# Performance work log

Measured on AMD Instinct MI355X. Metric: run time of the kernel, lower is better.

## Reference

```python
import jax, jax.numpy as jnp
import numpy as np

BITS = 8
BOUND = 2.0 ** (BITS - 1) - 1.0  # 127, symmetric int8 bound
EPS = 1e-6


def fake_quant(x, scale):
    """Symmetric fake quantization with straight-through estimator."""
    q = jnp.clip(jnp.round(x * scale), -BOUND, BOUND) / scale
    return x + jax.lax.stop_gradient(q - x)


def dense_aqt(x, w, b, mask):
    """AQT-style quantized dense: per-tensor input scale (masked stats),
    per-output-channel weight scale, int8-range fake quant, float GEMM.
    x: [N, Cin], w: [Cin, Cout], b: [Cout], mask: [N, 1]."""
    x_max = jnp.max(jnp.abs(x * mask))                       # masked per-tensor stat
    sx = BOUND / jnp.maximum(x_max, EPS)
    w_max = jnp.max(jnp.abs(w), axis=0, keepdims=True)        # [1, Cout]
    sw = BOUND / jnp.maximum(w_max, EPS)
    xq = fake_quant(x, sx)
    wq = fake_quant(w, sw)
    return jnp.matmul(xq, wq) + b


def setup_inputs() -> dict:
    key = jax.random.key(0)
    k1, k2, k3 = jax.random.split(key, 3)
    B, S, C, H = 4, 2048, 1024, 4096
    inputs = jax.random.normal(k1, (B, S, C), dtype=jnp.float32)
    padding_mask = jnp.ones((B, S, 1), dtype=jnp.float32)
    W1 = jax.random.normal(k2, (C, H), dtype=jnp.float32) * (1.0 / np.sqrt(C))
    b1 = jnp.zeros((H,), dtype=jnp.float32)
    W2 = jax.random.normal(k3, (H, C), dtype=jnp.float32) * (1.0 / np.sqrt(H))
    b2 = jnp.zeros((C,), dtype=jnp.float32)
    return {"inputs": inputs, "padding_mask": padding_mask,
            "W1": W1, "b1": b1, "W2": W2, "b2": b2}


def reference(inputs, padding_mask, W1, b1, W2, b2):
    B, S, C = inputs.shape
    x = inputs.reshape(B * S, C)
    m = padding_mask.reshape(B * S, 1)
    h = jax.nn.relu(dense_aqt(x, W1, b1, m))   # dropout is no-op (deterministic)
    out = dense_aqt(h, W2, b2, m)              # dropout is no-op (deterministic)
    return out.reshape(B, S, C)
```

## Files before the change

### kernel.cpp

```cpp
#include <hip/hip_runtime.h>
#include <hip/hip_fp16.h>
#include <stdint.h>


#define EPSQ 1e-6f
typedef int v4i __attribute__((ext_vector_type(4)));
typedef int v16i __attribute__((ext_vector_type(16)));

__device__ __forceinline__ void async16(const int8_t* g, int8_t* l) {
  __builtin_amdgcn_global_load_lds(
      (const __attribute__((address_space(1))) void*)g,
      (__attribute__((address_space(3))) void*)l, 16, 0, 0);
}
__device__ __forceinline__ unsigned short f2h(float f) {
  __half h = __float2half(f);
  return *(unsigned short*)&h;
}
__device__ __forceinline__ float4 max4(float4 m, float4 v) {
  m.x = fmaxf(m.x, fabsf(v.x)); m.y = fmaxf(m.y, fabsf(v.y));
  m.z = fmaxf(m.z, fabsf(v.z)); m.w = fmaxf(m.w, fabsf(v.w));
  return m;
}
__device__ __forceinline__ unsigned qmb(float x, float s) {
  return __float_as_uint(fmaf(x, s, 12582912.0f)) & 0xffu;
}
__device__ __forceinline__ unsigned q4f(float4 f, float s) {
  return qmb(f.x, s) | (qmb(f.y, s) << 8) | (qmb(f.z, s) << 16) |
         (__float_as_uint(fmaf(f.w, s, 12582912.0f)) << 24);
}
__device__ __forceinline__ unsigned q4h(unsigned ua, unsigned ub,
                                        __half2 s2, __half2 m2) {
  __half2 ha = __hfma2(*(__half2*)&ua, s2, m2);
  __half2 hb = __hfma2(*(__half2*)&ub, s2, m2);
  unsigned va = *(unsigned*)&ha, vb = *(unsigned*)&hb;
#if __has_builtin(__builtin_amdgcn_perm)
  return __builtin_amdgcn_perm(vb, va, 0x06040200u);
#else
  return (va & 0xffu) | ((va >> 8) & 0xff00u) |
         ((vb & 0xffu) << 16) | (((vb >> 8) & 0xff00u) << 16);
#endif
}

__global__ __launch_bounds__(256) void k_stats(
    const float* __restrict__ x, const float* __restrict__ mask,
    const float* __restrict__ W1, const float* __restrict__ W2,
    float* __restrict__ pmaxX, float* __restrict__ pcm1, float* __restrict__ pcm2) {
  const int bx = blockIdx.x, tid = threadIdx.x;
  if (bx < 64) {
    const int sp = bx & 15, cg = bx >> 4;
    const int col = cg * 1024 + tid * 4;
    float4 m = {0.f, 0.f, 0.f, 0.f};
#pragma unroll 8
    for (int r = 0; r < 64; ++r)
      m = max4(m, *(const float4*)(W1 + (size_t)(sp * 64 + r) * 4096 + col));
    *(float4*)(pcm1 + sp * 4096 + col) = m;
  } else if (bx < 128) {
    const int sp = bx - 64;
    const int col = tid * 4;
    float4 m = {0.f, 0.f, 0.f, 0.f};
#pragma unroll 8
    for (int r = 0; r < 64; ++r)
      m = max4(m, *(const float4*)(W2 + (size_t)(sp * 64 + r) * 1024 + col));
    *(float4*)(pcm2 + sp * 1024 + col) = m;
  } else {
    __shared__ float red[4];
    const int b = bx - 128;
    float lmax = 0.f;
    for (int c = b * 256 + tid; c < 1048576; c += 262144) {
      size_t idx = (size_t)c * 8;
      float mk = fabsf(mask[idx >> 10]);
      float4 m4 = {0.f, 0.f, 0.f, 0.f};
      m4 = max4(m4, *(const float4*)(x + idx));
      m4 = max4(m4, *(const float4*)(x + idx + 4));
      lmax = fmaxf(lmax, fmaxf(fmaxf(m4.x, m4.y), fmaxf(m4.z, m4.w)) * mk);
    }
    for (int s = 32; s; s >>= 1) lmax = fmaxf(lmax, __shfl_down(lmax, s));
    if ((tid & 63) == 0) red[tid >> 6] = lmax;
    __syncthreads();
    if (tid == 0)
      pmaxX[b] = fmaxf(fmaxf(red[0], red[1]), fmaxf(red[2], red[3]));
  }
}

__global__ __launch_bounds__(256) void k_quant(
    const float* __restrict__ x, const float* __restrict__ W1, const float* __restrict__ W2,
    const float* __restrict__ pmaxX, const float* __restrict__ pcm1, const float* __restrict__ pcm2,
    int8_t* __restrict__ qx, int8_t* __restrict__ qw1, int8_t* __restrict__ qw2,
    float* __restrict__ cm1, float* __restrict__ cm2, float* __restrict__ scG) {
  const int bx = blockIdx.x, tid = threadIdx.x;
  if (bx < 2048) {
    __shared__ float red[4];
    float v = fmaxf(fmaxf(pmaxX[tid], pmaxX[tid + 256]),
                    fmaxf(pmaxX[tid + 512], pmaxX[tid + 768]));
    for (int s = 32; s; s >>= 1) v = fmaxf(v, __shfl_down(v, s));
    if ((tid & 63) == 0) red[tid >> 6] = v;
    __syncthreads();
    const float xmax = fmaxf(fmaxf(red[0], red[1]), fmaxf(red[2], red[3]));
    if (bx == 0 && tid == 0) scG[0] = xmax;
    const float s = 127.0f / fmaxf(xmax, EPSQ);
    const int wave = tid >> 6, lane = tid & 63;
    const int f = bx * 4 + wave;
    const int r = (f >> 5) * 32 + (lane & 31);
    const int k = (f & 31) * 32 + (lane >> 5) * 16;
    const float4* src = (const float4*)(x + (size_t)r * 1024 + k);
    uint4 o;
    o.x = q4f(src[0], s); o.y = q4f(src[1], s);
    o.z = q4f(src[2], s); o.w = q4f(src[3], s);
    *(uint4*)(qx + (size_t)f * 1024 + lane * 16) = o;
  } else if (bx < 2304) {
    int id = (bx - 2048) * 256 + tid;
    int n4 = id & 1023, kc = id >> 10;
    const int col = n4 * 4;
    float4 cm = {0.f, 0.f, 0.f, 0.f};
#pragma unroll
    for (int sp = 0; sp < 16; ++sp) {
      float4 p = *(const float4*)(pcm1 + sp * 4096 + col);
      cm.x = fmaxf(cm.x, p.x); cm.y = fmaxf(cm.y, p.y);
      cm.z = fmaxf(cm.z, p.z); cm.w = fmaxf(cm.w, p.w);
    }
    if (kc == 0) *(float4*)(cm1 + col) = cm;
    const float s0 = 127.0f / fmaxf(cm.x, EPSQ), s1 = 127.0f / fmaxf(cm.y, EPSQ);
    const float s2 = 127.0f / fmaxf(cm.z, EPSQ), s3 = 127.0f / fmaxf(cm.w, EPSQ);
    union { int8_t p[16]; uint4 v; } u0, u1, u2, u3;
#pragma unroll
    for (int j = 0; j < 16; ++j) {
      float4 f = *(const float4*)(W1 + (size_t)(kc * 16 + j) * 4096 + col);
      u0.p[j] = (int8_t)qmb(f.x, s0); u1.p[j] = (int8_t)qmb(f.y, s1);
      u2.p[j] = (int8_t)qmb(f.z, s2); u3.p[j] = (int8_t)qmb(f.w, s3);
    }
    int8_t* base = qw1 + ((size_t)(col >> 5) * 32 + (kc >> 1)) * 1024 +
                   (kc & 1) * 512 + (col & 31) * 16;
    *(uint4*)(base) = u0.v;      *(uint4*)(base + 16) = u1.v;
    *(uint4*)(base + 32) = u2.v; *(uint4*)(base + 48) = u3.v;
  } else {
    int id = (bx - 2304) * 256 + tid;
    int n4 = id & 255, kc = id >> 8;
    const int col = n4 * 4;
    float4 cm = {0.f, 0.f, 0.f, 0.f};
#pragma unroll
    for (int sp = 0; sp < 64; ++sp) {
      float4 p = *(const float4*)(pcm2 + sp * 1024 + col);
      cm.x = fmaxf(cm.x, p.x); cm.y = fmaxf(cm.y, p.y);
      cm.z = fmaxf(cm.z, p.z); cm.w = fmaxf(cm.w, p.w);
    }
    if (kc == 0) *(float4*)(cm2 + col) = cm;
    const float s0 = 127.0f / fmaxf(cm.x, EPSQ), s1 = 127.0f / fmaxf(cm.y, EPSQ);
    const float s2 = 127.0f / fmaxf(cm.z, EPSQ), s3 = 127.0f / fmaxf(cm.w, EPSQ);
    union { int8_t p[16]; uint4 v; } u0, u1, u2, u3;
#pragma unroll
    for (int j = 0; j < 16; ++j) {
      float4 f = *(const float4*)(W2 + (size_t)(kc * 16 + j) * 1024 + col);
      u0.p[j] = (int8_t)qmb(f.x, s0); u1.p[j] = (int8_t)qmb(f.y, s1);
      u2.p[j] = (int8_t)qmb(f.z, s2); u3.p[j] = (int8_t)qmb(f.w, s3);
    }
    int8_t* base = qw2 + ((size_t)(col >> 5) * 128 + (kc >> 1)) * 1024 +
                   (kc & 1) * 512 + (col & 31) * 16;
    *(uint4*)(base) = u0.v;      *(uint4*)(base + 16) = u1.v;
    *(uint4*)(base + 32) = u2.v; *(uint4*)(base + 48) = u3.v;
  }
}

__global__ __launch_bounds__(512, 4) void gemm1(
    const int8_t* __restrict__ A, const int8_t* __restrict__ Bt,
    const float* __restrict__ sxp, const float* __restrict__ cmax,
    const float* __restrict__ bias, const float* __restrict__ mask,
    unsigned short* __restrict__ hfrag, float* __restrict__ pmaxH) {
  constexpr int NST = 16;
  constexpr int BUF = 24576;
  __shared__ __align__(16) int8_t smem[3 * BUF];
  const int tid = threadIdx.x;
  const int wave = tid >> 6, lane = tid & 63;

  const int bid = blockIdx.x;
  const int xcd = bid & 7, sl = bid >> 3;
  const int m0 = (xcd * 4 + (sl & 3)) * 256;
  const int n0 = (sl >> 2) * 128;

  v16i acc[2][2] = {};

  const int8_t* gA = A  + ((size_t)((m0 >> 5) + wave) * 32) * 1024 + lane * 16;
  const int8_t* gB = Bt + ((size_t)((n0 >> 5) + (wave & 3)) * 32 + (wave >> 2)) * 1024
                     + lane * 16;
  const int dAo = wave * 1024 + lane * 16;
  const int dBo = 16384 + ((wave >> 2) * 4 + (wave & 3)) * 1024 + lane * 16;

  async16(gA,        smem + dAo);
  async16(gA + 1024, smem + dAo + 8192);
  async16(gB,        smem + dBo);
  async16(gA + 2048, smem + BUF + dAo);
  async16(gA + 3072, smem + BUF + dAo + 8192);
  async16(gB + 2048, smem + BUF + dBo);
  asm volatile("s_waitcnt vmcnt(3)" ::: "memory");
  __builtin_amdgcn_s_barrier();
  __builtin_amdgcn_sched_barrier(0);

  const int mI = (wave & 3) * 2, nI = (wave >> 2) * 2;
#pragma unroll
  for (int kb = 0; kb < NST; ++kb) {
    const int co = (kb % 3) * BUF;
    if (kb + 2 < NST) {
      const int po = ((kb + 2) % 3) * BUF;
      async16(gA + (kb + 2) * 2048,        smem + po + dAo);
      async16(gA + (kb + 2) * 2048 + 1024, smem + po + dAo + 8192);
      async16(gB + (kb + 2) * 2048,        smem + po + dBo);
    }
    __builtin_amdgcn_sched_barrier(0);
#pragma unroll
    for (int kc = 0; kc < 2; ++kc) {
      v4i af0 = *(const v4i*)(smem + co + (kc * 8 + mI) * 1024 + lane * 16);
      v4i af1 = *(const v4i*)(smem + co + (kc * 8 + mI + 1) * 1024 + lane * 16);
      v4i bf0 = *(const v4i*)(smem + co + 16384 + (kc * 4 + nI) * 1024 + lane * 16);
      v4i bf1 = *(const v4i*)(smem + co + 16384 + (kc * 4 + nI + 1) * 1024 + lane * 16);
      acc[0][0] = __builtin_amdgcn_mfma_i32_32x32x32_i8(af0, bf0, acc[0][0], 0, 0, 0);
      acc[0][1] = __builtin_amdgcn_mfma_i32_32x32x32_i8(af0, bf1, acc[0][1], 0, 0, 0);
      acc[1][0] = __builtin_amdgcn_mfma_i32_32x32x32_i8(af1, bf0, acc[1][0], 0, 0, 0);
      acc[1][1] = __builtin_amdgcn_mfma_i32_32x32x32_i8(af1, bf1, acc[1][1], 0, 0, 0);
    }
    if (kb + 1 < NST) {
      asm volatile("s_waitcnt lgkmcnt(0)" ::: "memory");
      if (kb + 2 < NST)
        asm volatile("s_waitcnt vmcnt(3)" ::: "memory");
      else
        asm volatile("s_waitcnt vmcnt(0)" ::: "memory");
      __builtin_amdgcn_s_barrier();
      __builtin_amdgcn_sched_barrier(0);
    }
  }

  const float asc = fmaxf(sxp[0], EPSQ) * (1.0f / 127.0f);
  const int cl = lane & 31;
  const int rbase = 4 * (lane >> 5);
  const int wr = wave & 3, wc = wave >> 2;
  float bsc[2], bv[2];
#pragma unroll
  for (int nt = 0; nt < 2; ++nt) {
    const int col = n0 + wc * 64 + nt * 32 + cl;
    bsc[nt] = fmaxf(cmax[col], EPSQ) * (1.0f / 127.0f) * asc;
    bv[nt] = bias[col];
  }
  const int hwoff = (cl >> 4) * 512 + (cl & 15);
  float lmax = 0.f;
#pragma unroll
  for (int mt = 0; mt < 2; ++mt) {
    const int rowbase = m0 + wr * 64 + mt * 32;
    const size_t rowblk = (size_t)(rowbase >> 5);
#pragma unroll
    for (int g = 0; g < 4; ++g)
#pragma unroll
      for (int r2 = 0; r2 < 4; ++r2) {
        const int rloc = g * 8 + r2 + rbase;
        const float mk = fabsf(mask[rowbase + rloc]);
#pragma unroll
        for (int nt = 0; nt < 2; ++nt) {
          const size_t kblk = (size_t)((n0 + wc * 64 + nt * 32) >> 5);
          float v = (float)acc[mt][nt][g * 4 + r2] * bsc[nt] + bv[nt];
          v = fmaxf(v, 0.f);
          hfrag[(rowblk * 128 + kblk) * 1024 + hwoff + rloc * 16] = f2h(v);
          lmax = fmaxf(lmax, v * mk);
        }
      }
  }
  for (int s = 32; s; s >>= 1) lmax = fmaxf(lmax, __shfl_down(lmax, s));
  __syncthreads();
  float* redf = (float*)smem;
  if (lane == 0) redf[wave] = lmax;
  __syncthreads();
  if (tid == 0) {
    float r = redf[0];
#pragma unroll
    for (int j = 1; j < 8; ++j) r = fmaxf(r, redf[j]);
    pmaxH[bid] = r;
  }
}

__global__ __launch_bounds__(256, 2) void gemm2(
    const unsigned short* __restrict__ hfrag, const int8_t* __restrict__ Bt,
    const float* __restrict__ pmaxH, const float* __restrict__ cmax,
    const float* __restrict__ bias, float* __restrict__ out) {
  __shared__ __align__(16) int8_t smem[32768];
  int8_t* const lsA = smem;
  int8_t* const lsB = smem + 16384;
  const int tid = threadIdx.x;
  const int wave = tid >> 6, lane = tid & 63;

  float* red = (float*)smem;
  float v = 0.f;
#pragma unroll
  for (int j = 0; j < 4; ++j) v = fmaxf(v, pmaxH[tid + 256 * j]);
  for (int s = 32; s; s >>= 1) v = fmaxf(v, __shfl_down(v, s));
  if (lane == 0) red[wave] = v;
  __syncthreads();
  const float hmax = fmaxf(fmaxf(red[0], red[1]), fmaxf(red[2], red[3]));
  __syncthreads();
  const float asc = fmaxf(hmax, EPSQ) * (1.0f / 127.0f);
  const __half sh = __float2half_rn(127.0f / fmaxf(hmax, EPSQ));
  const __half2 s2 = __halves2half2(sh, sh);
  const __half mh = __float2half_rn(1536.0f);
  const __half2 m2 = __halves2half2(mh, mh);

  const int bid = blockIdx.x;
  const int xcd = bid & 7, slot = bid >> 3;
  const int m0 = ((xcd << 3) + (slot >> 3)) * 128;
  const int n0 = (slot & 7) * 128;

  v16i acc[2][2] = {};

  const uint4* hA = (const uint4*)hfrag;
  const size_t aBase = ((size_t)((m0 >> 5) + wave) * 128) * 128 + lane * 2;
  const int8_t* gB = Bt + ((size_t)((n0 >> 5) + wave) * 128) * 1024 + lane * 16;
  int8_t* const dA0 = lsA + (0 * 4 + wave) * 1024 + lane * 16;
  int8_t* const dA1 = lsA + (1 * 4 + wave) * 1024 + lane * 16;
  int8_t* const dB0 = lsB + (0 * 4 + wave) * 1024 + lane * 16;
  int8_t* const dB1 = lsB + (1 * 4 + wave) * 1024 + lane * 16;

  const int nsteps = 64;
  const int mI = (wave & 1) * 2, nI = (wave >> 1) * 2;

  uint4 s0a0 = {}, s0a1 = {}, s0c0 = {}, s0c1 = {};
  uint4 s1a0 = {}, s1a1 = {}, s1c0 = {}, s1c1 = {};

  {
    uint4 a0 = hA[aBase], a1 = hA[aBase + 1];
    uint4 c0 = hA[aBase + 128], c1 = hA[aBase + 129];
    async16(gB, dB0);
    async16(gB + 1024, dB1);
    __builtin_amdgcn_sched_barrier(0);
    s1a0 = hA[aBase + 2 * 128]; s1a1 = hA[aBase + 2 * 128 + 1];
    s1c0 = hA[aBase + 3 * 128]; s1c1 = hA[aBase + 3 * 128 + 1];
    uint4 o;
    o.x = q4h(a0.x, a0.y, s2, m2); o.y = q4h(a0.z, a0.w, s2, m2);
    o.z = q4h(a1.x, a1.y, s2, m2); o.w = q4h(a1.z, a1.w, s2, m2);
    *(uint4*)dA0 = o;
    o.x = q4h(c0.x, c0.y, s2, m2); o.y = q4h(c0.z, c0.w, s2, m2);
    o.z = q4h(c1.x, c1.y, s2, m2); o.w = q4h(c1.z, c1.w, s2, m2);
    *(uint4*)dA1 = o;
  }
  asm volatile("s_waitcnt lgkmcnt(0)" ::: "memory");
  asm volatile("s_waitcnt vmcnt(4)" ::: "memory");
  __builtin_amdgcn_s_barrier();
  __builtin_amdgcn_sched_barrier(0);

#pragma unroll 2
  for (int kb = 0; kb < nsteps; ++kb) {
    const int cur = kb & 1;
    const int co = cur * 8192, po = co ^ 8192;
    const bool more = (kb + 1 < nsteps);
    const bool deep = (kb + 2 < nsteps);
    if (more) {
      async16(gB + (size_t)((kb + 1) * 2) * 1024, dB0 + po);
      async16(gB + (size_t)((kb + 1) * 2 + 1) * 1024, dB1 + po);
      __builtin_amdgcn_sched_barrier(0);
      if (deep) {
        const size_t ai = aBase + (size_t)((kb + 2) * 2) * 128;
        if (cur) { s1a0 = hA[ai]; s1a1 = hA[ai + 1];
                   s1c0 = hA[ai + 128]; s1c1 = hA[ai + 129]; }
        else     { s0a0 = hA[ai]; s0a1 = hA[ai + 1];
                   s0c0 = hA[ai + 128]; s0c1 = hA[ai + 129]; }
      }
    }
#pragma unroll
    for (int kc = 0; kc < 2; ++kc) {
      v4i af0 = *(const v4i*)(lsA + co + (kc * 4 + mI) * 1024 + lane * 16);
      v4i af1 = *(const v4i*)(lsA + co + (kc * 4 + mI + 1) * 1024 + lane * 16);
      v4i bf0 = *(const v4i*)(lsB + co + (kc * 4 + nI) * 1024 + lane * 16);
      v4i bf1 = *(const v4i*)(lsB + co + (kc * 4 + nI + 1) * 1024 + lane * 16);
      acc[0][0] = __builtin_amdgcn_mfma_i32_32x32x32_i8(af0, bf0, acc[0][0], 0, 0, 0);
      acc[0][1] = __builtin_amdgcn_mfma_i32_32x32x32_i8(af0, bf1, acc[0][1], 0, 0, 0);
      acc[1][0] = __builtin_amdgcn_mfma_i32_32x32x32_i8(af1, bf0, acc[1][0], 0, 0, 0);
      acc[1][1] = __builtin_amdgcn_mfma_i32_32x32x32_i8(af1, bf1, acc[1][1], 0, 0, 0);
    }
    if (more) {
      const uint4 pa0 = cur ? s0a0 : s1a0, pa1 = cur ? s0a1 : s1a1;
      const uint4 pc0 = cur ? s0c0 : s1c0, pc1 = cur ? s0c1 : s1c1;
      uint4 o;
      o.x = q4h(pa0.x, pa0.y, s2, m2); o.y = q4h(pa0.z, pa0.w, s2, m2);
      o.z = q4h(pa1.x, pa1.y, s2, m2); o.w = q4h(pa1.z, pa1.w, s2, m2);
      *(uint4*)(dA0 + po) = o;
      o.x = q4h(pc0.x, pc0.y, s2, m2); o.y = q4h(pc0.z, pc0.w, s2, m2);
      o.z = q4h(pc1.x, pc1.y, s2, m2); o.w = q4h(pc1.z, pc1.w, s2, m2);
      *(uint4*)(dA1 + po) = o;
      asm volatile("s_waitcnt lgkmcnt(0)" ::: "memory");
      if (deep) asm volatile("s_waitcnt vmcnt(4)" ::: "memory");
      else      asm volatile("s_waitcnt vmcnt(0)" ::: "memory");
      __builtin_amdgcn_s_barrier();
      __builtin_amdgcn_sched_barrier(0);
    }
  }

  const int cl = lane & 31;
  const int rbase = 4 * (lane >> 5);
  const int wr = wave & 1, wc = wave >> 1;
  float bsc[2], bv[2];
  int colv[2];
#pragma unroll
  for (int nt = 0; nt < 2; ++nt) {
    colv[nt] = n0 + wc * 64 + nt * 32 + cl;
    bsc[nt] = fmaxf(cmax[colv[nt]], EPSQ) * (1.0f / 127.0f) * asc;
    bv[nt] = bias[colv[nt]];
  }
#pragma unroll
  for (int mt = 0; mt < 2; ++mt)
#pragma unroll
    for (int g = 0; g < 4; ++g)
#pragma unroll
      for (int r2 = 0; r2 < 4; ++r2) {
        const int row = m0 + wr * 64 + mt * 32 + g * 8 + r2 + rbase;
#pragma unroll
        for (int nt = 0; nt < 2; ++nt)
          out[(size_t)row * 1024 + colv[nt]] =
              (float)acc[mt][nt][g * 4 + r2] * bsc[nt] + bv[nt];
      }
}

extern "C" void kernel_launch(void* const* d_in, const int* in_sizes, int n_in,
                              void* d_out, int out_size, void* d_ws, size_t ws_size,
                              hipStream_t stream) {
  const float* x  = (const float*)d_in[0];
  const float* mk = (const float*)d_in[1];
  const float* W1 = (const float*)d_in[2];
  const float* b1 = (const float*)d_in[3];
  const float* W2 = (const float*)d_in[4];
  const float* b2 = (const float*)d_in[5];
  float* out = (float*)d_out;

  float* scG   = (float*)d_ws;
  float* pmaxX = scG + 8;
  float* pmaxH = pmaxX + 1024;
  float* pcm1  = pmaxH + 2048;
  float* pcm2  = pcm1 + 65536;
  float* cm1   = pcm2 + 65536;
  float* cm2   = cm1 + 4096;
  int8_t* qx  = (int8_t*)(cm2 + 1024);
  int8_t* qw1 = qx  + (size_t)8192 * 1024;
  int8_t* qw2 = qw1 + (size_t)4096 * 1024;
  unsigned short* h = (unsigned short*)(qw2 + (size_t)1024 * 4096);

  k_stats<<<1152, 256, 0, stream>>>(x, mk, W1, W2, pmaxX, pcm1, pcm2);
  k_quant<<<2560, 256, 0, stream>>>(x, W1, W2, pmaxX, pcm1, pcm2,
                                    qx, qw1, qw2, cm1, cm2, scG);
  gemm1<<<1024, 512, 0, stream>>>(qx, qw1, scG, cm1, b1, mk, h, pmaxH);
  gemm2<<<512, 256, 0, stream>>>(h, qw2, pmaxH, cm2, b2, out);
}
```

Measured before the change: 228.0 us.

## Deepen gemm2 pipeline to a four-stage LDS ring with split-phase barriers

The second int8 GEMM moves from double-buffered LDS to a four-slot ring. B tiles are prefetched two steps ahead via global_load_lds, and A activations are loaded into registers three steps ahead, then quantized into LDS two steps ahead. Each k-step is split into two halves with their own barrier, and the MFMA groups are wrapped in s_setprio. The aim is to hide global-load latency and barrier stalls behind MFMA work. In exchange, LDS per block grows to 64KB, which may limit occupancy, and the vmcnt ordering is implicit and fragile.

```diff
diff --git a/kernel.cpp b/kernel.cpp
--- a/kernel.cpp
+++ b/kernel.cpp
@@ -277,9 +277,8 @@
     const unsigned short* __restrict__ hfrag, const int8_t* __restrict__ Bt,
     const float* __restrict__ pmaxH, const float* __restrict__ cmax,
     const float* __restrict__ bias, float* __restrict__ out) {
-  __shared__ __align__(16) int8_t smem[32768];
-  int8_t* const lsA = smem;
-  int8_t* const lsB = smem + 16384;
+  constexpr int NST = 64;
+  __shared__ __align__(16) int8_t smem[4 * 16384];
   const int tid = threadIdx.x;
   const int wave = tid >> 6, lane = tid & 63;
 
@@ -308,81 +307,104 @@
   const uint4* hA = (const uint4*)hfrag;
   const size_t aBase = ((size_t)((m0 >> 5) + wave) * 128) * 128 + lane * 2;
   const int8_t* gB = Bt + ((size_t)((n0 >> 5) + wave) * 128) * 1024 + lane * 16;
-  int8_t* const dA0 = lsA + (0 * 4 + wave) * 1024 + lane * 16;
-  int8_t* const dA1 = lsA + (1 * 4 + wave) * 1024 + lane * 16;
-  int8_t* const dB0 = lsB + (0 * 4 + wave) * 1024 + lane * 16;
-  int8_t* const dB1 = lsB + (1 * 4 + wave) * 1024 + lane * 16;
-
-  const int nsteps = 64;
+  const int dA0o = (0 * 4 + wave) * 1024 + lane * 16;
+  const int dA1o = (1 * 4 + wave) * 1024 + lane * 16;
+  const int dB0o = 8192 + (0 * 4 + wave) * 1024 + lane * 16;
+  const int dB1o = 8192 + (1 * 4 + wave) * 1024 + lane * 16;
   const int mI = (wave & 1) * 2, nI = (wave >> 1) * 2;
 
-  uint4 s0a0 = {}, s0a1 = {}, s0c0 = {}, s0c1 = {};
-  uint4 s1a0 = {}, s1a1 = {}, s1c0 = {}, s1c1 = {};
+  uint4 ra0, ra1, rc0, rc1;
 
   {
     uint4 a0 = hA[aBase], a1 = hA[aBase + 1];
     uint4 c0 = hA[aBase + 128], c1 = hA[aBase + 129];
-    async16(gB, dB0);
-    async16(gB + 1024, dB1);
-    __builtin_amdgcn_sched_barrier(0);
-    s1a0 = hA[aBase + 2 * 128]; s1a1 = hA[aBase + 2 * 128 + 1];
-    s1c0 = hA[aBase + 3 * 128]; s1c1 = hA[aBase + 3 * 128 + 1];
+    __builtin_amdgcn_sched_barrier(0);
+    async16(gB,            smem + dB0o);
+    async16(gB + 1024,     smem + dB1o);
+    async16(gB + 2 * 1024, smem + 16384 + dB0o);
+    async16(gB + 3 * 1024, smem + 16384 + dB1o);
+    __builtin_amdgcn_sched_barrier(0);
     uint4 o;
     o.x = q4h(a0.x, a0.y, s2, m2); o.y = q4h(a0.z, a0.w, s2, m2);
     o.z = q4h(a1.x, a1.y, s2, m2); o.w = q4h(a1.z, a1.w, s2, m2);
-    *(uint4*)dA0 = o;
+    *(uint4*)(smem + dA0o) = o;
     o.x = q4h(c0.x, c0.y, s2, m2); o.y = q4h(c0.z, c0.w, s2, m2);
     o.z = q4h(c1.x, c1.y, s2, m2); o.w = q4h(c1.z, c1.w, s2, m2);
-    *(uint4*)dA1 = o;
+    *(uint4*)(smem + dA1o) = o;
+    __builtin_amdgcn_sched_barrier(0);
+    a0 = hA[aBase + 2 * 128]; a1 = hA[aBase + 2 * 128 + 1];
+    c0 = hA[aBase + 3 * 128]; c1 = hA[aBase + 3 * 128 + 1];
+    __builtin_amdgcn_sched_barrier(0);
+    o.x = q4h(a0.x, a0.y, s2, m2); o.y = q4h(a0.z, a0.w, s2, m2);
+    o.z = q4h(a1.x, a1.y, s2, m2); o.w = q4h(a1.z, a1.w, s2, m2);
+    *(uint4*)(smem + 16384 + dA0o) = o;
+    o.x = q4h(c0.x, c0.y, s2, m2); o.y = q4h(c0.z, c0.w, s2, m2);
+    o.z = q4h(c1.x, c1.y, s2, m2); o.w = q4h(c1.z, c1.w, s2, m2);
+    *(uint4*)(smem + 16384 + dA1o) = o;
+    __builtin_amdgcn_sched_barrier(0);
+    ra0 = hA[aBase + 4 * 128]; ra1 = hA[aBase + 4 * 128 + 1];
+    rc0 = hA[aBase + 5 * 128]; rc1 = hA[aBase + 5 * 128 + 1];
   }
   asm volatile("s_waitcnt lgkmcnt(0)" ::: "memory");
-  asm volatile("s_waitcnt vmcnt(4)" ::: "memory");
-  __builtin_amdgcn_s_barrier();
   __builtin_amdgcn_sched_barrier(0);
 
-#pragma unroll 2
-  for (int kb = 0; kb < nsteps; ++kb) {
-    const int cur = kb & 1;
-    const int co = cur * 8192, po = co ^ 8192;
-    const bool more = (kb + 1 < nsteps);
-    const bool deep = (kb + 2 < nsteps);
-    if (more) {
-      async16(gB + (size_t)((kb + 1) * 2) * 1024, dB0 + po);
-      async16(gB + (size_t)((kb + 1) * 2 + 1) * 1024, dB1 + po);
+#pragma unroll 4
+  for (int kb = 0; kb < NST; ++kb) {
+    const int cb = (kb & 3) * 16384;
+    const int nb2 = ((kb + 2) & 3) * 16384;
+    __builtin_amdgcn_s_barrier();
+    __builtin_amdgcn_sched_barrier(0);
+    {
+      v4i af0 = *(const v4i*)(smem + cb + (0 * 4 + mI) * 1024 + lane * 16);
+      v4i af1 = *(const v4i*)(smem + cb + (0 * 4 + mI + 1) * 1024 + lane * 16);
+      v4i bf0 = *(const v4i*)(smem + cb + 8192 + (0 * 4 + nI) * 1024 + lane * 16);
+      v4i bf1 = *(const v4i*)(smem + cb + 8192 + (0 * 4 + nI + 1) * 1024 + lane * 16);
+      if (kb + 2 < NST) {
+        async16(gB + (size_t)((kb + 2) * 2) * 1024,     smem + nb2 + dB0o);
+        async16(gB + (size_t)((kb + 2) * 2 + 1) * 1024, smem + nb2 + dB1o);
+      }
+      asm volatile("s_waitcnt lgkmcnt(0)" ::: "memory");
       __builtin_amdgcn_sched_barrier(0);
-      if (deep) {
-        const size_t ai = aBase + (size_t)((kb + 2) * 2) * 128;
-        if (cur) { s1a0 = hA[ai]; s1a1 = hA[ai + 1];
-                   s1c0 = hA[ai + 128]; s1c1 = hA[ai + 129]; }
-        else     { s0a0 = hA[ai]; s0a1 = hA[ai + 1];
-                   s0c0 = hA[ai + 128]; s0c1 = hA[ai + 129]; }
-      }
-    }
-#pragma unroll
-    for (int kc = 0; kc < 2; ++kc) {
-      v4i af0 = *(const v4i*)(lsA + co + (kc * 4 + mI) * 1024 + lane * 16);
-      v4i af1 = *(const v4i*)(lsA + co + (kc * 4 + mI + 1) * 1024 + lane * 16);
-      v4i bf0 = *(const v4i*)(lsB + co + (kc * 4 + nI) * 1024 + lane * 16);
-      v4i bf1 = *(const v4i*)(lsB + co + (kc * 4 + nI + 1) * 1024 + lane * 16);
+      __builtin_amdgcn_s_setprio(1);
       acc[0][0] = __builtin_amdgcn_mfma_i32_32x32x32_i8(af0, bf0, acc[0][0], 0, 0, 0);
       acc[0][1] = __builtin_amdgcn_mfma_i32_32x32x32_i8(af0, bf1, acc[0][1], 0, 0, 0);
       acc[1][0] = __builtin_amdgcn_mfma_i32_32x32x32_i8(af1, bf0, acc[1][0], 0, 0, 0);
       acc[1][1] = __builtin_amdgcn_mfma_i32_32x32x32_i8(af1, bf1, acc[1][1], 0, 0, 0);
-    }
-    if (more) {
-      const uint4 pa0 = cur ? s0a0 : s1a0, pa1 = cur ? s0a1 : s1a1;
-      const uint4 pc0 = cur ? s0c0 : s1c0, pc1 = cur ? s0c1 : s1c1;
-      uint4 o;
-      o.x = q4h(pa0.x, pa0.y, s2, m2); o.y = q4h(pa0.z, pa0.w, s2, m2);
-      o.z = q4h(pa1.x, pa1.y, s2, m2); o.w = q4h(pa1.z, pa1.w, s2, m2);
-      *(uint4*)(dA0 + po) = o;
-      o.x = q4h(pc0.x, pc0.y, s2, m2); o.y = q4h(pc0.z, pc0.w, s2, m2);
-      o.z = q4h(pc1.x, pc1.y, s2, m2); o.w = q4h(pc1.z, pc1.w, s2, m2);
-      *(uint4*)(dA1 + po) = o;
+      __builtin_amdgcn_s_setprio(0);
+      __builtin_amdgcn_sched_barrier(0);
+    }
+    __builtin_amdgcn_s_barrier();
+    __builtin_amdgcn_sched_barrier(0);
+    {
+      v4i af0 = *(const v4i*)(smem + cb + (1 * 4 + mI) * 1024 + lane * 16);
+      v4i af1 = *(const v4i*)(smem + cb + (1 * 4 + mI + 1) * 1024 + lane * 16);
+      v4i bf0 = *(const v4i*)(smem + cb + 8192 + (1 * 4 + nI) * 1024 + lane * 16);
+      v4i bf1 = *(const v4i*)(smem + cb + 8192 + (1 * 4 + nI + 1) * 1024 + lane * 16);
+      if (kb + 2 < NST) {
+        uint4 o;
+        o.x = q4h(ra0.x, ra0.y, s2, m2); o.y = q4h(ra0.z, ra0.w, s2, m2);
+        o.z = q4h(ra1.x, ra1.y, s2, m2); o.w = q4h(ra1.z, ra1.w, s2, m2);
+        *(uint4*)(smem + nb2 + dA0o) = o;
+        o.x = q4h(rc0.x, rc0.y, s2, m2); o.y = q4h(rc0.z, rc0.w, s2, m2);
+        o.z = q4h(rc1.x, rc1.y, s2, m2); o.w = q4h(rc1.z, rc1.w, s2, m2);
+        *(uint4*)(smem + nb2 + dA1o) = o;
+        __builtin_amdgcn_sched_barrier(0);
+        if (kb + 3 < NST) {
+          const size_t ai = aBase + (size_t)((kb + 3) * 2) * 128;
+          ra0 = hA[ai]; ra1 = hA[ai + 1];
+          rc0 = hA[ai + 128]; rc1 = hA[ai + 129];
+        }
+      } else {
+        asm volatile("s_waitcnt vmcnt(0)" ::: "memory");
+      }
       asm volatile("s_waitcnt lgkmcnt(0)" ::: "memory");
-      if (deep) asm volatile("s_waitcnt vmcnt(4)" ::: "memory");
-      else      asm volatile("s_waitcnt vmcnt(0)" ::: "memory");
-      __builtin_amdgcn_s_barrier();
+      __builtin_amdgcn_sched_barrier(0);
+      __builtin_amdgcn_s_setprio(1);
+      acc[0][0] = __builtin_amdgcn_mfma_i32_32x32x32_i8(af0, bf0, acc[0][0], 0, 0, 0);
+      acc[0][1] = __builtin_amdgcn_mfma_i32_32x32x32_i8(af0, bf1, acc[0][1], 0, 0, 0);
+      acc[1][0] = __builtin_amdgcn_mfma_i32_32x32x32_i8(af1, bf0, acc[1][0], 0, 0, 0);
+      acc[1][1] = __builtin_amdgcn_mfma_i32_32x32x32_i8(af1, bf1, acc[1][1], 0, 0, 0);
+      __builtin_amdgcn_s_setprio(0);
       __builtin_amdgcn_sched_barrier(0);
     }
   }
```

Result: no change. 229.9 us (+0.8%).

## Load A fragments straight to registers, stage only B in LDS

Applied to the files above, without the earlier changes.

In both GEMM kernels, each wave now loads its A-operand fragments directly from global memory into registers, double-buffered across k-steps. Only the shared B tile is staged in LDS, which shrinks LDS use and removes the A LDS writes and reads and their lgkm waits. gemm2 now quantizes its fp16 A fragments in registers right before the MFMAs and gives each wave a 32x128 strip, with occupancy raised to 3 blocks. s_setprio hints wrap the MFMA groups. The trade-off is more register pressure and no LDS sharing of A, which is fine because each A fragment is used by a single wave.

```diff
diff --git a/kernel.cpp b/kernel.cpp
--- a/kernel.cpp
+++ b/kernel.cpp
@@ -166,8 +166,7 @@
     const float* __restrict__ bias, const float* __restrict__ mask,
     unsigned short* __restrict__ hfrag, float* __restrict__ pmaxH) {
   constexpr int NST = 16;
-  constexpr int BUF = 24576;
-  __shared__ __align__(16) int8_t smem[3 * BUF];
+  __shared__ __align__(16) int8_t smem[2 * 8192];
   const int tid = threadIdx.x;
   const int wave = tid >> 6, lane = tid & 63;
 
@@ -175,53 +174,69 @@
   const int xcd = bid & 7, sl = bid >> 3;
   const int m0 = (xcd * 4 + (sl & 3)) * 256;
   const int n0 = (sl >> 2) * 128;
+  const int wr = wave & 3, wc = wave >> 2;
 
   v16i acc[2][2] = {};
 
-  const int8_t* gA = A  + ((size_t)((m0 >> 5) + wave) * 32) * 1024 + lane * 16;
-  const int8_t* gB = Bt + ((size_t)((n0 >> 5) + (wave & 3)) * 32 + (wave >> 2)) * 1024
-                     + lane * 16;
-  const int dAo = wave * 1024 + lane * 16;
-  const int dBo = 16384 + ((wave >> 2) * 4 + (wave & 3)) * 1024 + lane * 16;
-
-  async16(gA,        smem + dAo);
-  async16(gA + 1024, smem + dAo + 8192);
-  async16(gB,        smem + dBo);
-  async16(gA + 2048, smem + BUF + dAo);
-  async16(gA + 3072, smem + BUF + dAo + 8192);
-  async16(gB + 2048, smem + BUF + dBo);
-  asm volatile("s_waitcnt vmcnt(3)" ::: "memory");
+  const int8_t* gA = A + ((size_t)((m0 >> 5) + wr * 2) * 32) * 1024 + lane * 16;
+  const int kcS = wave >> 2, nbS = wave & 3;
+  const int8_t* gB = Bt + ((size_t)((n0 >> 5) + nbS) * 32 + kcS) * 1024 + lane * 16;
+  const int dBo = wave * 1024 + lane * 16;
+  const int rdo = wc * 2048 + lane * 16;
+
+  v4i aP0, aP1, aP2, aP3, aQ0, aQ1, aQ2, aQ3;
+
+  async16(gB, smem + dBo);
+  __builtin_amdgcn_sched_barrier(0);
+  aP0 = *(const v4i*)(gA);
+  aP1 = *(const v4i*)(gA + 1024);
+  aP2 = *(const v4i*)(gA + 32768);
+  aP3 = *(const v4i*)(gA + 32768 + 1024);
+  asm volatile("s_waitcnt vmcnt(4)" ::: "memory");
   __builtin_amdgcn_s_barrier();
   __builtin_amdgcn_sched_barrier(0);
 
-  const int mI = (wave & 3) * 2, nI = (wave >> 2) * 2;
-#pragma unroll
+#pragma unroll 2
   for (int kb = 0; kb < NST; ++kb) {
-    const int co = (kb % 3) * BUF;
-    if (kb + 2 < NST) {
-      const int po = ((kb + 2) % 3) * BUF;
-      async16(gA + (kb + 2) * 2048,        smem + po + dAo);
-      async16(gA + (kb + 2) * 2048 + 1024, smem + po + dAo + 8192);
-      async16(gB + (kb + 2) * 2048,        smem + po + dBo);
-    }
-    __builtin_amdgcn_sched_barrier(0);
-#pragma unroll
-    for (int kc = 0; kc < 2; ++kc) {
-      v4i af0 = *(const v4i*)(smem + co + (kc * 8 + mI) * 1024 + lane * 16);
-      v4i af1 = *(const v4i*)(smem + co + (kc * 8 + mI + 1) * 1024 + lane * 16);
-      v4i bf0 = *(const v4i*)(smem + co + 16384 + (kc * 4 + nI) * 1024 + lane * 16);
-      v4i bf1 = *(const v4i*)(smem + co + 16384 + (kc * 4 + nI + 1) * 1024 + lane * 16);
-      acc[0][0] = __builtin_amdgcn_mfma_i32_32x32x32_i8(af0, bf0, acc[0][0], 0, 0, 0);
-      acc[0][1] = __builtin_amdgcn_mfma_i32_32x32x32_i8(af0, bf1, acc[0][1], 0, 0, 0);
-      acc[1][0] = __builtin_amdgcn_mfma_i32_32x32x32_i8(af1, bf0, acc[1][0], 0, 0, 0);
-      acc[1][1] = __builtin_amdgcn_mfma_i32_32x32x32_i8(af1, bf1, acc[1][1], 0, 0, 0);
-    }
-    if (kb + 1 < NST) {
-      asm volatile("s_waitcnt lgkmcnt(0)" ::: "memory");
-      if (kb + 2 < NST)
-        asm volatile("s_waitcnt vmcnt(3)" ::: "memory");
-      else
-        asm volatile("s_waitcnt vmcnt(0)" ::: "memory");
+    const int slot = (kb & 1) * 8192, nslot = slot ^ 8192;
+    const bool more = (kb + 1 < NST);
+    if (more) {
+      async16(gB + (size_t)(kb + 1) * 2048, smem + nslot + dBo);
+      __builtin_amdgcn_sched_barrier(0);
+      const int8_t* ga = gA + (size_t)(kb + 1) * 2048;
+      if (kb & 1) {
+        aP0 = *(const v4i*)(ga);         aP1 = *(const v4i*)(ga + 1024);
+        aP2 = *(const v4i*)(ga + 32768); aP3 = *(const v4i*)(ga + 32768 + 1024);
+      } else {
+        aQ0 = *(const v4i*)(ga);         aQ1 = *(const v4i*)(ga + 1024);
+        aQ2 = *(const v4i*)(ga + 32768); aQ3 = *(const v4i*)(ga + 32768 + 1024);
+      }
+      __builtin_amdgcn_sched_barrier(0);
+    }
+    {
+      const v4i a00 = (kb & 1) ? aQ0 : aP0;
+      const v4i a01 = (kb & 1) ? aQ1 : aP1;
+      const v4i a10 = (kb & 1) ? aQ2 : aP2;
+      const v4i a11 = (kb & 1) ? aQ3 : aP3;
+      v4i b0 = *(const v4i*)(smem + slot + rdo);
+      v4i b1 = *(const v4i*)(smem + slot + rdo + 1024);
+      __builtin_amdgcn_s_setprio(1);
+      acc[0][0] = __builtin_amdgcn_mfma_i32_32x32x32_i8(a00, b0, acc[0][0], 0, 0, 0);
+      acc[0][1] = __builtin_amdgcn_mfma_i32_32x32x32_i8(a00, b1, acc[0][1], 0, 0, 0);
+      acc[1][0] = __builtin_amdgcn_mfma_i32_32x32x32_i8(a10, b0, acc[1][0], 0, 0, 0);
+      acc[1][1] = __builtin_amdgcn_mfma_i32_32x32x32_i8(a10, b1, acc[1][1], 0, 0, 0);
+      __builtin_amdgcn_s_setprio(0);
+      v4i b2 = *(const v4i*)(smem + slot + 4096 + rdo);
+      v4i b3 = *(const v4i*)(smem + slot + 4096 + rdo + 1024);
+      __builtin_amdgcn_s_setprio(1);
+      acc[0][0] = __builtin_amdgcn_mfma_i32_32x32x32_i8(a01, b2, acc[0][0], 0, 0, 0);
+      acc[0][1] = __builtin_amdgcn_mfma_i32_32x32x32_i8(a01, b3, acc[0][1], 0, 0, 0);
+      acc[1][0] = __builtin_amdgcn_mfma_i32_32x32x32_i8(a11, b2, acc[1][0], 0, 0, 0);
+      acc[1][1] = __builtin_amdgcn_mfma_i32_32x32x32_i8(a11, b3, acc[1][1], 0, 0, 0);
+      __builtin_amdgcn_s_setprio(0);
+    }
+    if (more) {
+      asm volatile("s_waitcnt vmcnt(4)" ::: "memory");
       __builtin_amdgcn_s_barrier();
       __builtin_amdgcn_sched_barrier(0);
     }
@@ -230,7 +245,6 @@
   const float asc = fmaxf(sxp[0], EPSQ) * (1.0f / 127.0f);
   const int cl = lane & 31;
   const int rbase = 4 * (lane >> 5);
-  const int wr = wave & 3, wc = wave >> 2;
   float bsc[2], bv[2];
 #pragma unroll
   for (int nt = 0; nt < 2; ++nt) {
@@ -273,13 +287,12 @@
   }
 }
 
-__global__ __launch_bounds__(256, 2) void gemm2(
+__global__ __launch_bounds__(256, 3) void gemm2(
     const unsigned short* __restrict__ hfrag, const int8_t* __restrict__ Bt,
     const float* __restrict__ pmaxH, const float* __restrict__ cmax,
     const float* __restrict__ bias, float* __restrict__ out) {
-  __shared__ __align__(16) int8_t smem[32768];
-  int8_t* const lsA = smem;
-  int8_t* const lsB = smem + 16384;
+  constexpr int NST = 64;
+  __shared__ __align__(16) int8_t smem[2 * 8192];
   const int tid = threadIdx.x;
   const int wave = tid >> 6, lane = tid & 63;
 
@@ -299,89 +312,83 @@
   const __half2 m2 = __halves2half2(mh, mh);
 
   const int bid = blockIdx.x;
-  const int xcd = bid & 7, slot = bid >> 3;
-  const int m0 = ((xcd << 3) + (slot >> 3)) * 128;
-  const int n0 = (slot & 7) * 128;
-
-  v16i acc[2][2] = {};
+  const int xcd = bid & 7, slot2 = bid >> 3;
+  const int m0 = ((xcd << 3) + (slot2 >> 3)) * 128;
+  const int n0 = (slot2 & 7) * 128;
+
+  v16i acc[4] = {};
 
   const uint4* hA = (const uint4*)hfrag;
-  const size_t aBase = ((size_t)((m0 >> 5) + wave) * 128) * 128 + lane * 2;
+  const size_t aBase = ((size_t)((m0 >> 5) + wave) * 128) * 128 + (size_t)lane * 2;
   const int8_t* gB = Bt + ((size_t)((n0 >> 5) + wave) * 128) * 1024 + lane * 16;
-  int8_t* const dA0 = lsA + (0 * 4 + wave) * 1024 + lane * 16;
-  int8_t* const dA1 = lsA + (1 * 4 + wave) * 1024 + lane * 16;
-  int8_t* const dB0 = lsB + (0 * 4 + wave) * 1024 + lane * 16;
-  int8_t* const dB1 = lsB + (1 * 4 + wave) * 1024 + lane * 16;
-
-  const int nsteps = 64;
-  const int mI = (wave & 1) * 2, nI = (wave >> 1) * 2;
-
-  uint4 s0a0 = {}, s0a1 = {}, s0c0 = {}, s0c1 = {};
-  uint4 s1a0 = {}, s1a1 = {}, s1c0 = {}, s1c1 = {};
-
-  {
-    uint4 a0 = hA[aBase], a1 = hA[aBase + 1];
-    uint4 c0 = hA[aBase + 128], c1 = hA[aBase + 129];
-    async16(gB, dB0);
-    async16(gB + 1024, dB1);
-    __builtin_amdgcn_sched_barrier(0);
-    s1a0 = hA[aBase + 2 * 128]; s1a1 = hA[aBase + 2 * 128 + 1];
-    s1c0 = hA[aBase + 3 * 128]; s1c1 = hA[aBase + 3 * 128 + 1];
-    uint4 o;
-    o.x = q4h(a0.x, a0.y, s2, m2); o.y = q4h(a0.z, a0.w, s2, m2);
-    o.z = q4h(a1.x, a1.y, s2, m2); o.w = q4h(a1.z, a1.w, s2, m2);
-    *(uint4*)dA0 = o;
-    o.x = q4h(c0.x, c0.y, s2, m2); o.y = q4h(c0.z, c0.w, s2, m2);
-    o.z = q4h(c1.x, c1.y, s2, m2); o.w = q4h(c1.z, c1.w, s2, m2);
-    *(uint4*)dA1 = o;
-  }
-  asm volatile("s_waitcnt lgkmcnt(0)" ::: "memory");
+  const int dB0o = wave * 1024 + lane * 16;
+  const int dB1o = (4 + wave) * 1024 + lane * 16;
+  const int rdo = lane * 16;
+
+  uint4 hP0, hP1, hP2, hP3, hQ0, hQ1, hQ2, hQ3;
+
+  async16(gB, smem + dB0o);
+  async16(gB + 1024, smem + dB1o);
+  __builtin_amdgcn_sched_barrier(0);
+  hP0 = hA[aBase];       hP1 = hA[aBase + 1];
+  hP2 = hA[aBase + 128]; hP3 = hA[aBase + 129];
   asm volatile("s_waitcnt vmcnt(4)" ::: "memory");
   __builtin_amdgcn_s_barrier();
   __builtin_amdgcn_sched_barrier(0);
 
 #pragma unroll 2
-  for (int kb = 0; kb < nsteps; ++kb) {
-    const int cur = kb & 1;
-    const int co = cur * 8192, po = co ^ 8192;
-    const bool more = (kb + 1 < nsteps);
-    const bool deep = (kb + 2 < nsteps);
+  for (int kb = 0; kb < NST; ++kb) {
+    const int slot = (kb & 1) * 8192, nslot = slot ^ 8192;
+    const bool more = (kb + 1 < NST);
     if (more) {
-      async16(gB + (size_t)((kb + 1) * 2) * 1024, dB0 + po);
-      async16(gB + (size_t)((kb + 1) * 2 + 1) * 1024, dB1 + po);
-      __builtin_amdgcn_sched_barrier(0);
-      if (deep) {
-        const size_t ai = aBase + (size_t)((kb + 2) * 2) * 128;
-        if (cur) { s1a0 = hA[ai]; s1a1 = hA[ai + 1];
-                   s1c0 = hA[ai + 128]; s1c1 = hA[ai + 129]; }
-        else     { s0a0 = hA[ai]; s0a1 = hA[ai + 1];
-                   s0c0 = hA[ai + 128]; s0c1 = hA[ai + 129]; }
+      async16(gB + (size_t)((kb + 1) * 2) * 1024,     smem + nslot + dB0o);
+      async16(gB + (size_t)((kb + 1) * 2 + 1) * 1024, smem + nslot + dB1o);
+      __builtin_amdgcn_sched_barrier(0);
+      const size_t ai = aBase + (size_t)((kb + 1) * 2) * 128;
+      if (kb & 1) {
+        hP0 = hA[ai];       hP1 = hA[ai + 1];
+        hP2 = hA[ai + 128]; hP3 = hA[ai + 129];
+      } else {
+        hQ0 = hA[ai];       hQ1 = hA[ai + 1];
+        hQ2 = hA[ai + 128]; hQ3 = hA[ai + 129];
       }
-    }
-#pragma unroll
-    for (int kc = 0; kc < 2; ++kc) {
-      v4i af0 = *(const v4i*)(lsA + co + (kc * 4 + mI) * 1024 + lane * 16);
-      v4i af1 = *(const v4i*)(lsA + co + (kc * 4 + mI + 1) * 1024 + lane * 16);
-      v4i bf0 = *(const v4i*)(lsB + co + (kc * 4 + nI) * 1024 + lane * 16);
-      v4i bf1 = *(const v4i*)(lsB + co + (kc * 4 + nI + 1) * 1024 + lane * 16);
-      acc[0][0] = __builtin_amdgcn_mfma_i32_32x32x32_i8(af0, bf0, acc[0][0], 0, 0, 0);
-      acc[0][1] = __builtin_amdgcn_mfma_i32_32x32x32_i8(af0, bf1, acc[0][1], 0, 0, 0);
-      acc[1][0] = __builtin_amdgcn_mfma_i32_32x32x32_i8(af1, bf0, acc[1][0], 0, 0, 0);
-      acc[1][1] = __builtin_amdgcn_mfma_i32_32x32x32_i8(af1, bf1, acc[1][1], 0, 0, 0);
+      __builtin_amdgcn_sched_barrier(0);
+    }
+    {
+      const uint4 h0 = (kb & 1) ? hQ0 : hP0;
+      const uint4 h1 = (kb & 1) ? hQ1 : hP1;
+      const uint4 h2 = (kb & 1) ? hQ2 : hP2;
+      const uint4 h3 = (kb & 1) ? hQ3 : hP3;
+      uint4 oa, ob;
+      oa.x = q4h(h0.x, h0.y, s2, m2); oa.y = q4h(h0.z, h0.w, s2, m2);
+      oa.z = q4h(h1.x, h1.y, s2, m2); oa.w = q4h(h1.z, h1.w, s2, m2);
+      ob.x = q4h(h2.x, h2.y, s2, m2); ob.y = q4h(h2.z, h2.w, s2, m2);
+      ob.z = q4h(h3.x, h3.y, s2, m2); ob.w = q4h(h3.z, h3.w, s2, m2);
+      const v4i af0 = *(const v4i*)&oa;
+      const v4i af1 = *(const v4i*)&ob;
+      v4i b0 = *(const v4i*)(smem + slot + rdo);
+      v4i b1 = *(const v4i*)(smem + slot + 1024 + rdo);
+      v4i b2 = *(const v4i*)(smem + slot + 2048 + rdo);
+      v4i b3 = *(const v4i*)(smem + slot + 3072 + rdo);
+      __builtin_amdgcn_s_setprio(1);
+      acc[0] = __builtin_amdgcn_mfma_i32_32x32x32_i8(af0, b0, acc[0], 0, 0, 0);
+      acc[1] = __builtin_amdgcn_mfma_i32_32x32x32_i8(af0, b1, acc[1], 0, 0, 0);
+      acc[2] = __builtin_amdgcn_mfma_i32_32x32x32_i8(af0, b2, acc[2], 0, 0, 0);
+      acc[3] = __builtin_amdgcn_mfma_i32_32x32x32_i8(af0, b3, acc[3], 0, 0, 0);
+      __builtin_amdgcn_s_setprio(0);
+      b0 = *(const v4i*)(smem + slot + 4096 + rdo);
+      b1 = *(const v4i*)(smem + slot + 5120 + rdo);
+      b2 = *(const v4i*)(smem + slot + 6144 + rdo);
+      b3 = *(const v4i*)(smem + slot + 7168 + rdo);
+      __builtin_amdgcn_s_setprio(1);
+      acc[0] = __builtin_amdgcn_mfma_i32_32x32x32_i8(af1, b0, acc[0], 0, 0, 0);
+      acc[1] = __builtin_amdgcn_mfma_i32_32x32x32_i8(af1, b1, acc[1], 0, 0, 0);
+      acc[2] = __builtin_amdgcn_mfma_i32_32x32x32_i8(af1, b2, acc[2], 0, 0, 0);
+      acc[3] = __builtin_amdgcn_mfma_i32_32x32x32_i8(af1, b3, acc[3], 0, 0, 0);
+      __builtin_amdgcn_s_setprio(0);
     }
     if (more) {
-      const uint4 pa0 = cur ? s0a0 : s1a0, pa1 = cur ? s0a1 : s1a1;
-      const uint4 pc0 = cur ? s0c0 : s1c0, pc1 = cur ? s0c1 : s1c1;
-      uint4 o;
-      o.x = q4h(pa0.x, pa0.y, s2, m2); o.y = q4h(pa0.z, pa0.w, s2, m2);
-      o.z = q4h(pa1.x, pa1.y, s2, m2); o.w = q4h(pa1.z, pa1.w, s2, m2);
-      *(uint4*)(dA0 + po) = o;
-      o.x = q4h(pc0.x, pc0.y, s2, m2); o.y = q4h(pc0.z, pc0.w, s2, m2);
-      o.z = q4h(pc1.x, pc1.y, s2, m2); o.w = q4h(pc1.z, pc1.w, s2, m2);
-      *(uint4*)(dA1 + po) = o;
-      asm volatile("s_waitcnt lgkmcnt(0)" ::: "memory");
-      if (deep) asm volatile("s_waitcnt vmcnt(4)" ::: "memory");
-      else      asm volatile("s_waitcnt vmcnt(0)" ::: "memory");
+      asm volatile("s_waitcnt vmcnt(4)" ::: "memory");
       __builtin_amdgcn_s_barrier();
       __builtin_amdgcn_sched_barrier(0);
     }
@@ -389,27 +396,24 @@
 
   const int cl = lane & 31;
   const int rbase = 4 * (lane >> 5);
-  const int wr = wave & 1, wc = wave >> 1;
-  float bsc[2], bv[2];
-  int colv[2];
-#pragma unroll
-  for (int nt = 0; nt < 2; ++nt) {
-    colv[nt] = n0 + wc * 64 + nt * 32 + cl;
-    bsc[nt] = fmaxf(cmax[colv[nt]], EPSQ) * (1.0f / 127.0f) * asc;
-    bv[nt] = bias[colv[nt]];
-  }
-#pragma unroll
-  for (int mt = 0; mt < 2; ++mt)
-#pragma unroll
-    for (int g = 0; g < 4; ++g)
-#pragma unroll
-      for (int r2 = 0; r2 < 4; ++r2) {
-        const int row = m0 + wr * 64 + mt * 32 + g * 8 + r2 + rbase;
-#pragma unroll
-        for (int nt = 0; nt < 2; ++nt)
-          out[(size_t)row * 1024 + colv[nt]] =
-              (float)acc[mt][nt][g * 4 + r2] * bsc[nt] + bv[nt];
-      }
+  float bsc[4], bv[4];
+  int colv[4];
+#pragma unroll
+  for (int nf = 0; nf < 4; ++nf) {
+    colv[nf] = n0 + nf * 32 + cl;
+    bsc[nf] = fmaxf(cmax[colv[nf]], EPSQ) * (1.0f / 127.0f) * asc;
+    bv[nf] = bias[colv[nf]];
+  }
+#pragma unroll
+  for (int g = 0; g < 4; ++g)
+#pragma unroll
+    for (int r2 = 0; r2 < 4; ++r2) {
+      const int row = m0 + wave * 32 + g * 8 + r2 + rbase;
+#pragma unroll
+      for (int nf = 0; nf < 4; ++nf)
+        out[(size_t)row * 1024 + colv[nf]] =
+            (float)acc[nf][g * 4 + r2] * bsc[nf] + bv[nf];
+    }
 }
 
 extern "C" void kernel_launch(void* const* d_in, const int* in_sizes, int n_in,
```

Measured after the change: 225.4 us. No clear change (-1.1%).
